# Performance work log

Hardware: AMD Instinct MI355X
Metric: run time of the kernel (lower is better)

The kernel has to match this reference:

```python
import jax, jax.numpy as jnp
import numpy as np

B, S, HID, NH, HD = 2, 2048, 1024, 16, 64  # batch, seq, hidden, heads, head_dim (1024//NH)
ROPE_THETA = 10000.0
EPS = 1e-5


def _ternary_quantize(w):
    # BitNet b1.58 absmean weight quantization: ternary values + scalar scale.
    s = jnp.mean(jnp.abs(w)) + EPS
    q = jnp.clip(jnp.round(w / s), -1.0, 1.0)
    return q, s


def _rotate_half(x):
    x1, x2 = jnp.split(x, 2, axis=-1)
    return jnp.concatenate((-x2, x1), axis=-1)


def _rope_cos_sin(position_ids, head_dim, dtype):
    inv_freq = 1.0 / (ROPE_THETA ** (jnp.arange(0, head_dim, 2, dtype=jnp.float32) / head_dim))
    freqs = position_ids.astype(jnp.float32)[..., None] * inv_freq  # [b, s, hd/2]
    emb = jnp.concatenate((freqs, freqs), axis=-1)  # [b, s, hd]
    # add head axis -> [b, 1, s, hd]
    return jnp.cos(emb)[:, None].astype(dtype), jnp.sin(emb)[:, None].astype(dtype)


def setup_inputs() -> dict:
    key = jax.random.key(0)
    ks = jax.random.split(key, 5)
    hidden_states = jax.random.normal(ks[0], (B, S, HID), jnp.float32)
    hidden_states_scale = jnp.ones((1,), jnp.float32)
    position_ids = jnp.broadcast_to(jnp.arange(S, dtype=jnp.int32), (B, S))
    wq = jax.random.normal(ks[1], (HID, HID), jnp.float32) * 0.02
    wk = jax.random.normal(ks[2], (HID, HID), jnp.float32) * 0.02
    wv = jax.random.normal(ks[3], (HID, HID), jnp.float32) * 0.02
    wo = jax.random.normal(ks[4], (HID, HID), jnp.float32) * 0.02
    return {"hidden_states": hidden_states, "hidden_states_scale": hidden_states_scale,
            "position_ids": position_ids, "wq": wq, "wk": wk, "wv": wv, "wo": wo}


def reference(hidden_states, hidden_states_scale, position_ids, wq, wk, wv, wo):
    b, s, _ = hidden_states.shape
    hs_scale = hidden_states_scale.reshape(())

    # QuantizedLinear: ternary weight values, scale carried separately.
    wq_q, sq = _ternary_quantize(wq)
    wk_q, sk = _ternary_quantize(wk)
    wv_q, sv = _ternary_quantize(wv)
    wo_q, so = _ternary_quantize(wo)

    # Projections in the quantized-value domain: out = x @ Wq^T, out_scale = x_scale * w_scale
    q = jnp.einsum('bsh,oh->bso', hidden_states, wq_q)
    k = jnp.einsum('bsh,oh->bso', hidden_states, wk_q)
    v = jnp.einsum('bsh,oh->bso', hidden_states, wv_q)
    q_scale = hs_scale * sq
    k_scale = hs_scale * sk
    v_scale = hs_scale * sv

    # [b, nh, s, hd]
    q = q.reshape(b, s, NH, HD).transpose(0, 2, 1, 3)
    k = k.reshape(b, s, NH, HD).transpose(0, 2, 1, 3)
    v = v.reshape(b, s, NH, HD).transpose(0, 2, 1, 3)

    cos, sin = _rope_cos_sin(position_ids, HD, q.dtype)
    q = q * cos + _rotate_half(q) * sin
    k = k * cos + _rotate_half(k) * sin

    # quantized_matmul(Q, qs, K, ks): values multiply, scales multiply (scale unused by softmax,
    # matching the original which softmaxes the quantized-domain scores).
    attn = jnp.einsum('bhqd,bhkd->bhqk', q, k).astype(jnp.float32) * (1.0 / np.sqrt(HD))
    attn = jax.nn.softmax(attn, axis=-1)

    # quantized_matmul(attn, 1.0, V, vs)
    out = jnp.einsum('bhqk,bhkd->bhqd', attn, v.astype(jnp.float32))
    out_scale = 1.0 * v_scale

    out = out.transpose(0, 2, 1, 3).reshape(b, s, HID)
    out = jnp.einsum('bsh,oh->bso', out, wo_q)
    out_scale = out_scale * so
    return out, out_scale
```

## Files before the change

kernel.cpp:

```cpp
#include <hip/hip_runtime.h>
#include <hip/hip_bf16.h>

#define NB 2
#define NS 2048
#define NHID 1024
#define NHEAD 16
#define NHD 64
#define NTOK (NB*NS)
#define WELEM (NHID*NHID)

typedef unsigned short u16;
typedef __attribute__((ext_vector_type(4))) float floatx4;
typedef __attribute__((ext_vector_type(16))) float floatx16;
typedef __attribute__((ext_vector_type(8))) __bf16 bf16x8;
typedef __attribute__((ext_vector_type(8))) unsigned short ushort8;
typedef __attribute__((ext_vector_type(4))) unsigned short ushort4v;
typedef __attribute__((ext_vector_type(2))) unsigned uint2v;

__device__ __forceinline__ u16 f2bf(float f) {
  union { float f; unsigned u; } a; a.f = f;
  unsigned u = a.u;
  unsigned r = (u + 0x7fffu + ((u >> 16) & 1u)) >> 16;
  return (u16)r;
}
__device__ __forceinline__ float bf2f(u16 s) {
  union { unsigned u; float f; } a; a.u = ((unsigned)s) << 16;
  return a.f;
}
__device__ __forceinline__ void gload16(const void* g, void* lds) {
  __builtin_amdgcn_global_load_lds(
      (const __attribute__((address_space(1))) unsigned int*)g,
      (__attribute__((address_space(3))) unsigned int*)lds, 16, 0, 0);
}
__device__ __forceinline__ uint2v pl32(unsigned a, unsigned b) {
  return __builtin_amdgcn_permlane32_swap(a, b, false, false);
}
__device__ __forceinline__ float mergemax(float x) {
  uint2v r = pl32(__float_as_uint(x), __float_as_uint(x));
  return fmaxf(__uint_as_float(r[0]), __uint_as_float(r[1]));
}
__device__ __forceinline__ float tmax16(const floatx16& v) {
  float a = fmaxf(fmaxf(v[0], v[1]), v[2]);
  float b = fmaxf(fmaxf(v[3], v[4]), v[5]);
  float c = fmaxf(fmaxf(v[6], v[7]), v[8]);
  float d = fmaxf(fmaxf(v[9], v[10]), v[11]);
  float e = fmaxf(fmaxf(v[12], v[13]), v[14]);
  float r0 = fmaxf(fmaxf(a, b), c);
  float r1 = fmaxf(fmaxf(d, e), v[15]);
  return fmaxf(r0, r1);
}

__global__ void k_abssum(const float* __restrict__ wq, const float* __restrict__ wk,
                         const float* __restrict__ wv, const float* __restrict__ wo,
                         double* __restrict__ sums) {
  const float* srcs[4] = {wq, wk, wv, wo};
  const float* w = srcs[blockIdx.y];
  int idx = (blockIdx.x * 256 + threadIdx.x) * 16;
  float s = 0.f;
#pragma unroll
  for (int j = 0; j < 4; j++) {
    float4 v = *(const float4*)(w + idx + j * 4);
    s += fabsf(v.x) + fabsf(v.y) + fabsf(v.z) + fabsf(v.w);
  }
#pragma unroll
  for (int off = 32; off; off >>= 1) s += __shfl_down(s, off);
  __shared__ float ps[4];
  if ((threadIdx.x & 63) == 0) ps[threadIdx.x >> 6] = s;
  __syncthreads();
  if (threadIdx.x == 0) atomicAdd(&sums[blockIdx.y], (double)(ps[0] + ps[1] + ps[2] + ps[3]));
}

__global__ void k_quantsplit(const float* __restrict__ wq, const float* __restrict__ wk,
                             const float* __restrict__ wv, const float* __restrict__ wo,
                             const double* __restrict__ sums, u16* __restrict__ wt,
                             const float* __restrict__ x,
                             u16* __restrict__ xh, u16* __restrict__ xl,
                             float2* __restrict__ rtab) {
  int bid = blockIdx.x;
  if (bid < 4096) {
    const float* srcs[4] = {wq, wk, wv, wo};
    int y = bid >> 10, xb = bid & 1023;
    const float* w = srcs[y];
    u16* dst = wt + y * WELEM;
    float s = (float)(sums[y] / (double)WELEM) + 1e-5f;
    int idx = (xb * 256 + threadIdx.x) * 4;
    float4 v = *(const float4*)(w + idx);
    float f[4] = {v.x, v.y, v.z, v.w};
    union { u16 ss[4]; uint2 u; } O;
#pragma unroll
    for (int j = 0; j < 4; j++) {
      float q = rintf(f[j] / s);
      q = fminf(1.f, fmaxf(-1.f, q));
      O.ss[j] = f2bf(q);
    }
    *(uint2*)(dst + idx) = O.u;
  } else if (bid < 8192) {
    int idx = ((bid - 4096) * 256 + threadIdx.x) * 4;
    float4 v = *(const float4*)(x + idx);
    float f[4] = {v.x, v.y, v.z, v.w};
    union { u16 s[4]; uint2 u; } H, L;
#pragma unroll
    for (int j = 0; j < 4; j++) {
      u16 hb = f2bf(f[j]);
      H.s[j] = hb;
      L.s[j] = f2bf(f[j] - bf2f(hb));
    }
    *(uint2*)(xh + idx) = H.u;
    *(uint2*)(xl + idx) = L.u;
  } else {
    int idx = (bid - 8192) * 256 + threadIdx.x;
    int d = idx & 31;
    float p = (float)(idx >> 5);
    float inv = exp2f((float)d * -0.4152410118609203f);
    float fr = p * inv;
    rtab[idx] = make_float2(cosf(fr), sinf(fr));
  }
}

template <int MODE>
__global__ __launch_bounds__(256) void k_gemm(
    const u16* __restrict__ Ahi, const u16* __restrict__ Alo,
    const u16* __restrict__ Wt, const int* __restrict__ pos_ids,
    const float2* __restrict__ rtab, float* __restrict__ outf,
    u16* __restrict__ qh, u16* __restrict__ ql,
    u16* __restrict__ kh, u16* __restrict__ kl,
    u16* __restrict__ vt,
    const double* __restrict__ sums, const float* __restrict__ hss) {
  constexpr int BUF = (MODE == 0) ? 24576 : 16384;
  __shared__ __attribute__((aligned(16))) char GSM[2 * BUF];
  const int tid = threadIdx.x;
  const int wave = tid >> 6, lane = tid & 63;
  const int lr = lane & 15, lh = lane >> 4;
  const int bm = blockIdx.x, bn = blockIdx.y, z = blockIdx.z;
  const u16* W = Wt + (MODE == 0 ? z : 3) * WELEM;
  const int wr = wave >> 1, wc = wave & 1;

  floatx4 acc[4][4];
#pragma unroll
  for (int i = 0; i < 4; i++)
#pragma unroll
    for (int j = 0; j < 4; j++) acc[i][j] = (floatx4){0.f, 0.f, 0.f, 0.f};

  const int e0 = tid * 8;
  const int row0 = e0 >> 5, col0 = e0 & 31;

  auto stage = [&](int k0, int nb) {
#pragma unroll
    for (int it = 0; it < 2; ++it) {
      int row = row0 + it * 64;
      gload16(Ahi + (bm * 128 + row) * 1024 + k0 + col0, GSM + nb + it * 4096 + wave * 1024);
      if (MODE == 0 && z != 2)
        gload16(Alo + (bm * 128 + row) * 1024 + k0 + col0, GSM + nb + 8192 + it * 4096 + wave * 1024);
      gload16(W + (bn * 128 + row) * 1024 + k0 + col0,
              GSM + nb + (MODE == 0 ? 16384 : 8192) + it * 4096 + wave * 1024);
    }
  };

  stage(0, 0);

  for (int kt = 0; kt < 32; ++kt) {
    __syncthreads();
    const int cb = (kt & 1) * BUF;
    if (kt < 31) stage((kt + 1) * 32, ((kt + 1) & 1) * BUF);

    const u16* Ahp = (const u16*)(GSM + cb);
    const u16* Bp  = (const u16*)(GSM + cb + (MODE == 0 ? 16384 : 8192));
    bf16x8 ah[4], bfr[4];
#pragma unroll
    for (int mi = 0; mi < 4; mi++)
      ah[mi] = *(const bf16x8*)(Ahp + (wr * 64 + mi * 16 + lr) * 32 + lh * 8);
#pragma unroll
    for (int ni = 0; ni < 4; ni++)
      bfr[ni] = *(const bf16x8*)(Bp + (wc * 64 + ni * 16 + lr) * 32 + lh * 8);
#pragma unroll
    for (int mi = 0; mi < 4; mi++)
#pragma unroll
      for (int ni = 0; ni < 4; ni++)
        acc[mi][ni] = __builtin_amdgcn_mfma_f32_16x16x32_bf16(ah[mi], bfr[ni], acc[mi][ni], 0, 0, 0);
    if (MODE == 0 && z != 2) {
      const u16* Alp = (const u16*)(GSM + cb + 8192);
      bf16x8 al8[4];
#pragma unroll
      for (int mi = 0; mi < 4; mi++)
        al8[mi] = *(const bf16x8*)(Alp + (wr * 64 + mi * 16 + lr) * 32 + lh * 8);
#pragma unroll
      for (int mi = 0; mi < 4; mi++)
#pragma unroll
        for (int ni = 0; ni < 4; ni++)
          acc[mi][ni] = __builtin_amdgcn_mfma_f32_16x16x32_bf16(al8[mi], bfr[ni], acc[mi][ni], 0, 0, 0);
    }
  }

  if (MODE == 1) {
#pragma unroll
    for (int mi = 0; mi < 4; mi++)
#pragma unroll
      for (int ni = 0; ni < 4; ni++)
#pragma unroll
        for (int i = 0; i < 4; i++) {
          int row = bm * 128 + wr * 64 + mi * 16 + lh * 4 + i;
          int col = bn * 128 + wc * 64 + ni * 16 + lr;
          outf[row * 1024 + col] = acc[mi][ni][i];
        }
    if (bm == 0 && bn == 0 && tid == 0) {
      float sv = (float)(sums[2] / (double)WELEM) + 1e-5f;
      float so = (float)(sums[3] / (double)WELEM) + 1e-5f;
      outf[NTOK * NHID] = hss[0] * sv * so;
    }
    return;
  }

  const int hh = bn * 2 + wc;
  if (z == 2) {
#pragma unroll
    for (int mi = 0; mi < 4; mi++) {
      int row0v = bm * 128 + wr * 64 + mi * 16 + lh * 4;
      int bb = row0v >> 11, s_ = row0v & 2047;
      size_t vbase = ((size_t)(bb * NHEAD + hh)) * (NHD * NS) + s_;
#pragma unroll
      for (int ni = 0; ni < 4; ni++) {
        int hd = ni * 16 + lr;
        union { u16 s4[4]; ushort4v v; } V4;
#pragma unroll
        for (int i = 0; i < 4; i++) V4.s4[i] = f2bf(acc[mi][ni][i]);
        *(ushort4v*)(vt + vbase + (size_t)hd * NS) = V4.v;
      }
    }
    return;
  }

  const float qsc = (z == 0) ? 0.125f * 1.4426950408889634f : 1.0f;
  u16* dh = z ? kh : qh;
  u16* dl = z ? kl : ql;
  int posr[4][4];
#pragma unroll
  for (int mi = 0; mi < 4; mi++)
#pragma unroll
    for (int i = 0; i < 4; i++) {
      int row = bm * 128 + wr * 64 + mi * 16 + lh * 4 + i;
      posr[mi][i] = pos_ids[(row >> 11) * NS + (row & 2047)];
    }
#pragma unroll
  for (int ni = 0; ni < 2; ni++) {
    int d = ni * 16 + lr;
#pragma unroll
    for (int mi = 0; mi < 4; mi++)
#pragma unroll
      for (int i = 0; i < 4; i++) {
        int row = bm * 128 + wr * 64 + mi * 16 + lh * 4 + i;
        int bb = row >> 11, s_ = row & 2047;
        float2 cs = rtab[posr[mi][i] * 32 + d];
        float x1 = acc[mi][ni][i], x2 = acc[mi][ni + 2][i];
        float n1 = (x1 * cs.x - x2 * cs.y) * qsc;
        float n2 = (x2 * cs.x + x1 * cs.y) * qsc;
        size_t ob = ((size_t)(bb * NHEAD + hh) * NS + s_) * NHD + d;
        u16 h1 = f2bf(n1);
        dh[ob] = h1;      dl[ob] = f2bf(n1 - bf2f(h1));
        u16 h2 = f2bf(n2);
        dh[ob + 32] = h2; dl[ob + 32] = f2bf(n2 - bf2f(h2));
      }
  }
}

__global__ __launch_bounds__(512) void k_attn(
    const u16* __restrict__ qh, const u16* __restrict__ ql,
    const u16* __restrict__ kh, const u16* __restrict__ kl,
    const u16* __restrict__ vt, u16* __restrict__ aoh) {
  __shared__ __attribute__((aligned(16))) char SM[98304];
  const int tid = threadIdx.x, wave = tid >> 6, lane = tid & 63;
  const int l5 = lane & 31, hi = lane >> 5;
  const int bid = blockIdx.x;
  const int swzb = ((bid & 7) << 5) | (bid >> 3);
  const int qt = swzb & 7, bh = swzb >> 3;
  const int b = bh >> 4, hco = (bh & 15) * NHD;
  const int base = bh * (NS * NHD);
  const int qrow = qt * 256 + wave * 32 + l5;

  bf16x8 qfh[4], qfl[4];
#pragma unroll
  for (int s = 0; s < 4; s++) {
    int off = base + qrow * NHD + s * 16 + hi * 8;
    qfh[s] = *(const bf16x8*)(qh + off);
    qfl[s] = *(const bf16x8*)(ql + off);
  }
  union { ushort8 u; bf16x8 v; } ONES;
#pragma unroll
  for (int j = 0; j < 8; j++) ONES.u[j] = 0x3F80;

  const floatx16 Z16 = {};
  floatx16 acco[2], accl;
  acco[0] = Z16; acco[1] = Z16; accl = Z16;
  float m_r = -1e30f;

  const char* khg0 = (const char*)(kh + base);
  const char* klg0 = (const char*)(kl + base);
  const char* vtg0 = (const char*)(vt + base);

#define STAGE_KV(key0_, nb_)                                                     \
  {                                                                              \
    const char* khg = khg0 + (key0_) * 128;                                      \
    const char* klg = klg0 + (key0_) * 128;                                      \
    const char* vtg = vtg0 + (key0_) * 2;                                        \
    _Pragma("unroll")                                                            \
    for (int it = 0; it < 2; ++it) {                                             \
      int L = it * 8192 + tid * 16;                                              \
      int r7 = (L >> 7) & 7;                                                     \
      int g = L ^ (r7 << 4);                                                     \
      int dst = (nb_) + it * 8192 + wave * 1024;                                 \
      gload16(khg + g, SM + dst);                                                \
      gload16(klg + g, SM + 16384 + dst);                                        \
      int vcol = (L & 255) ^ (((L >> 8) & 15) << 4);                             \
      gload16(vtg + (size_t)(L >> 8) * 4096 + vcol, SM + 32768 + dst);           \
    }                                                                            \
  }

  STAGE_KV(0, 0);

  for (int kt = 0; kt < 16; ++kt) {
    __syncthreads();
    const int cb = (kt & 1) * 49152;
    const int key0 = kt * 128;

    if (kt < 15) STAGE_KV(key0 + 128, ((kt + 1) & 1) * 49152);

    floatx16 sacc[4];
#pragma unroll
    for (int t = 0; t < 4; t++) {
      const int row = 32 * t + l5;
      const int swz = (row & 7) << 4;
      {
        int byt = cb + row * 128 + ((hi * 16) ^ swz);
        bf16x8 ah = *(const bf16x8*)(SM + byt);
        bf16x8 al8 = *(const bf16x8*)(SM + 16384 + byt);
        __builtin_amdgcn_s_setprio(1);
        sacc[t] = __builtin_amdgcn_mfma_f32_32x32x16_bf16(ah, qfh[0], Z16, 0, 0, 0);
        sacc[t] = __builtin_amdgcn_mfma_f32_32x32x16_bf16(ah, qfl[0], sacc[t], 0, 0, 0);
        sacc[t] = __builtin_amdgcn_mfma_f32_32x32x16_bf16(al8, qfh[0], sacc[t], 0, 0, 0);
        __builtin_amdgcn_s_setprio(0);
      }
#pragma unroll
      for (int s = 1; s < 4; s++) {
        int byt = cb + row * 128 + ((s * 32 + hi * 16) ^ swz);
        bf16x8 ah = *(const bf16x8*)(SM + byt);
        bf16x8 al8 = *(const bf16x8*)(SM + 16384 + byt);
        __builtin_amdgcn_s_setprio(1);
        sacc[t] = __builtin_amdgcn_mfma_f32_32x32x16_bf16(ah, qfh[s], sacc[t], 0, 0, 0);
        sacc[t] = __builtin_amdgcn_mfma_f32_32x32x16_bf16(ah, qfl[s], sacc[t], 0, 0, 0);
        sacc[t] = __builtin_amdgcn_mfma_f32_32x32x16_bf16(al8, qfh[s], sacc[t], 0, 0, 0);
        __builtin_amdgcn_s_setprio(0);
      }
    }

    float mt = fmaxf(fmaxf(tmax16(sacc[0]), tmax16(sacc[1])),
                     fmaxf(tmax16(sacc[2]), tmax16(sacc[3])));
    mt = mergemax(mt);
    if (!__all(mt <= m_r + 8.0f)) {
      float mn = fmaxf(m_r, mt);
      float sc2 = exp2f(m_r - mn);
      accl[0] *= sc2;
#pragma unroll
      for (int dt = 0; dt < 2; dt++)
#pragma unroll
        for (int r = 0; r < 16; r++) acco[dt][r] *= sc2;
      m_r = mn;
    }
#pragma unroll
    for (int t = 0; t < 4; t++)
#pragma unroll
      for (int r = 0; r < 16; r++)
        sacc[t][r] = exp2f(sacc[t][r] - m_r);

#pragma unroll
    for (int s = 0; s < 8; s++) {
      int t = s >> 1, rb = (s & 1) * 8;
      union { __bf16 bb[8]; unsigned u[4]; } Wp;
#pragma unroll
      for (int j = 0; j < 8; j++) Wp.bb[j] = (__bf16)sacc[t][rb + j];
      uint2v r02 = pl32(Wp.u[0], Wp.u[2]);
      uint2v r13 = pl32(Wp.u[1], Wp.u[3]);
      union { unsigned u[4]; bf16x8 v; } P;
      P.u[0] = r02[0]; P.u[1] = r13[0]; P.u[2] = r02[1]; P.u[3] = r13[1];
      const int coloff = (s * 32 + hi * 16) ^ ((l5 & 15) << 4);
      bf16x8 v0 = *(const bf16x8*)(SM + cb + 32768 + l5 * 256 + coloff);
      bf16x8 v1 = *(const bf16x8*)(SM + cb + 32768 + (l5 + 32) * 256 + coloff);
      __builtin_amdgcn_s_setprio(1);
      acco[0] = __builtin_amdgcn_mfma_f32_32x32x16_bf16(v0, P.v, acco[0], 0, 0, 0);
      acco[1] = __builtin_amdgcn_mfma_f32_32x32x16_bf16(v1, P.v, acco[1], 0, 0, 0);
      accl    = __builtin_amdgcn_mfma_f32_32x32x16_bf16(ONES.v, P.v, accl, 0, 0, 0);
      __builtin_amdgcn_s_setprio(0);
    }
  }

  float inv = 1.0f / accl[0];
  float* OT = (float*)SM;
#pragma unroll
  for (int rnd = 0; rnd < 2; rnd++) {
    __syncthreads();
    if ((wave >> 2) == rnd) {
      int orow = (wave & 3) * 32 + l5;
#pragma unroll
      for (int dt = 0; dt < 2; dt++)
#pragma unroll
        for (int r = 0; r < 16; r++) {
          int col = (r & 3) + 8 * (r >> 2) + 4 * hi + 32 * dt;
          int cs = (col & 32) | ((col ^ l5) & 31);
          OT[orow * 64 + cs] = acco[dt][r] * inv;
        }
    }
    __syncthreads();
    {
      int row = tid >> 2, q4 = tid & 3;
      union { u16 s8[8]; ushort8 v; } HB[2];
#pragma unroll
      for (int j = 0; j < 16; j++) {
        int c = q4 * 16 + j;
        int cs = (c & 32) | ((c ^ (row & 31)) & 31);
        HB[j >> 3].s8[j & 7] = f2bf(OT[row * 64 + cs]);
      }
      int rowg = qt * 256 + rnd * 128 + row;
      size_t doff = ((size_t)(b * NS + rowg)) * NHID + hco + q4 * 16;
      *(ushort8*)(aoh + doff) = HB[0].v;
      *(ushort8*)(aoh + doff + 8) = HB[1].v;
    }
  }
}

extern "C" void kernel_launch(void* const* d_in, const int* in_sizes, int n_in,
                              void* d_out, int out_size, void* d_ws, size_t ws_size,
                              hipStream_t stream) {
  const float* x   = (const float*)d_in[0];
  const float* hss = (const float*)d_in[1];
  const int*   pos = (const int*)d_in[2];
  const float* wq  = (const float*)d_in[3];
  const float* wk  = (const float*)d_in[4];
  const float* wv  = (const float*)d_in[5];
  const float* wo  = (const float*)d_in[6];
  float* out = (float*)d_out;
  char* ws = (char*)d_ws;
  const size_t MB = 1u << 20;
  u16* wt = (u16*)(ws);
  u16* xh = (u16*)(ws + 8 * MB);
  u16* xl = (u16*)(ws + 16 * MB);
  u16* qh = (u16*)(ws + 24 * MB);
  u16* ql = (u16*)(ws + 32 * MB);
  u16* kh = (u16*)(ws + 40 * MB);
  u16* kl = (u16*)(ws + 48 * MB);
  u16* vt = (u16*)(ws + 56 * MB);
  double* sums = (double*)(ws + 72 * MB);
  float2* rtab = (float2*)(ws + 73 * MB);
  u16* aoh = xh;

  hipMemsetAsync(sums, 0, 4 * sizeof(double), stream);
  k_abssum<<<dim3(256, 4), 256, 0, stream>>>(wq, wk, wv, wo, sums);
  k_quantsplit<<<8448, 256, 0, stream>>>(wq, wk, wv, wo, sums, wt, x, xh, xl, rtab);
  k_gemm<0><<<dim3(32, 8, 3), 256, 0, stream>>>(xh, xl, wt, pos, rtab, nullptr,
                                                qh, ql, kh, kl, vt, nullptr, nullptr);
  k_attn<<<256, 512, 0, stream>>>(qh, ql, kh, kl, vt, aoh);
  k_gemm<1><<<dim3(32, 8, 1), 256, 0, stream>>>(aoh, nullptr, wt, nullptr, nullptr, out,
                                                nullptr, nullptr, nullptr, nullptr, nullptr,
                                                sums, hss);
}
```

Measured before the change: 192.7 us.

## Software-pipeline attention with 64-key tiles and triple-buffered LDS

New measurement: 194.6 us. About the same (+1.0%).

```diff
diff --git a/kernel.cpp b/kernel.cpp
--- a/kernel.cpp
+++ b/kernel.cpp
@@ -266,7 +266,7 @@
     const u16* __restrict__ qh, const u16* __restrict__ ql,
     const u16* __restrict__ kh, const u16* __restrict__ kl,
     const u16* __restrict__ vt, u16* __restrict__ aoh) {
-  __shared__ __attribute__((aligned(16))) char SM[98304];
+  __shared__ __attribute__((aligned(16))) char SM[73728];
   const int tid = threadIdx.x, wave = tid >> 6, lane = tid & 63;
   const int l5 = lane & 31, hi = lane >> 5;
   const int bid = blockIdx.x;
@@ -301,58 +301,46 @@
     const char* khg = khg0 + (key0_) * 128;                                      \
     const char* klg = klg0 + (key0_) * 128;                                      \
     const char* vtg = vtg0 + (key0_) * 2;                                        \
-    _Pragma("unroll")                                                            \
-    for (int it = 0; it < 2; ++it) {                                             \
-      int L = it * 8192 + tid * 16;                                              \
-      int r7 = (L >> 7) & 7;                                                     \
-      int g = L ^ (r7 << 4);                                                     \
-      int dst = (nb_) + it * 8192 + wave * 1024;                                 \
-      gload16(khg + g, SM + dst);                                                \
-      gload16(klg + g, SM + 16384 + dst);                                        \
-      int vcol = (L & 255) ^ (((L >> 8) & 15) << 4);                             \
-      gload16(vtg + (size_t)(L >> 8) * 4096 + vcol, SM + 32768 + dst);           \
-    }                                                                            \
-  }
-
-  STAGE_KV(0, 0);
-
-  for (int kt = 0; kt < 16; ++kt) {
-    __syncthreads();
-    const int cb = (kt & 1) * 49152;
-    const int key0 = kt * 128;
-
-    if (kt < 15) STAGE_KV(key0 + 128, ((kt + 1) & 1) * 49152);
-
-    floatx16 sacc[4];
-#pragma unroll
-    for (int t = 0; t < 4; t++) {
+    int L = tid * 16;                                                            \
+    int r7 = (L >> 7) & 7;                                                       \
+    int g = L ^ (r7 << 4);                                                       \
+    gload16(khg + g, SM + (nb_) + wave * 1024);                                  \
+    gload16(klg + g, SM + (nb_) + 8192 + wave * 1024);                           \
+    int vcol = (L & 127) ^ (r7 << 4);                                            \
+    gload16(vtg + (size_t)(L >> 7) * 4096 + vcol, SM + (nb_) + 16384 + wave * 1024); \
+  }
+
+  auto QK = [&](floatx16 (&sc)[2], int kbuf) {
+#pragma unroll
+    for (int t = 0; t < 2; t++) {
       const int row = 32 * t + l5;
       const int swz = (row & 7) << 4;
       {
-        int byt = cb + row * 128 + ((hi * 16) ^ swz);
+        int byt = kbuf + row * 128 + ((hi * 16) ^ swz);
         bf16x8 ah = *(const bf16x8*)(SM + byt);
-        bf16x8 al8 = *(const bf16x8*)(SM + 16384 + byt);
+        bf16x8 al8 = *(const bf16x8*)(SM + 8192 + byt);
         __builtin_amdgcn_s_setprio(1);
-        sacc[t] = __builtin_amdgcn_mfma_f32_32x32x16_bf16(ah, qfh[0], Z16, 0, 0, 0);
-        sacc[t] = __builtin_amdgcn_mfma_f32_32x32x16_bf16(ah, qfl[0], sacc[t], 0, 0, 0);
-        sacc[t] = __builtin_amdgcn_mfma_f32_32x32x16_bf16(al8, qfh[0], sacc[t], 0, 0, 0);
+        sc[t] = __builtin_amdgcn_mfma_f32_32x32x16_bf16(ah, qfh[0], Z16, 0, 0, 0);
+        sc[t] = __builtin_amdgcn_mfma_f32_32x32x16_bf16(ah, qfl[0], sc[t], 0, 0, 0);
+        sc[t] = __builtin_amdgcn_mfma_f32_32x32x16_bf16(al8, qfh[0], sc[t], 0, 0, 0);
         __builtin_amdgcn_s_setprio(0);
       }
 #pragma unroll
       for (int s = 1; s < 4; s++) {
-        int byt = cb + row * 128 + ((s * 32 + hi * 16) ^ swz);
+        int byt = kbuf + row * 128 + ((s * 32 + hi * 16) ^ swz);
         bf16x8 ah = *(const bf16x8*)(SM + byt);
-        bf16x8 al8 = *(const bf16x8*)(SM + 16384 + byt);
+        bf16x8 al8 = *(const bf16x8*)(SM + 8192 + byt);
         __builtin_amdgcn_s_setprio(1);
-        sacc[t] = __builtin_amdgcn_mfma_f32_32x32x16_bf16(ah, qfh[s], sacc[t], 0, 0, 0);
-        sacc[t] = __builtin_amdgcn_mfma_f32_32x32x16_bf16(ah, qfl[s], sacc[t], 0, 0, 0);
-        sacc[t] = __builtin_amdgcn_mfma_f32_32x32x16_bf16(al8, qfh[s], sacc[t], 0, 0, 0);
+        sc[t] = __builtin_amdgcn_mfma_f32_32x32x16_bf16(ah, qfh[s], sc[t], 0, 0, 0);
+        sc[t] = __builtin_amdgcn_mfma_f32_32x32x16_bf16(ah, qfl[s], sc[t], 0, 0, 0);
+        sc[t] = __builtin_amdgcn_mfma_f32_32x32x16_bf16(al8, qfh[s], sc[t], 0, 0, 0);
         __builtin_amdgcn_s_setprio(0);
       }
     }
-
-    float mt = fmaxf(fmaxf(tmax16(sacc[0]), tmax16(sacc[1])),
-                     fmaxf(tmax16(sacc[2]), tmax16(sacc[3])));
+  };
+
+  auto SMPV = [&](floatx16 (&sc)[2], int vbuf) {
+    float mt = fmaxf(tmax16(sc[0]), tmax16(sc[1]));
     mt = mergemax(mt);
     if (!__all(mt <= m_r + 8.0f)) {
       float mn = fmaxf(m_r, mt);
@@ -365,30 +353,53 @@
       m_r = mn;
     }
 #pragma unroll
-    for (int t = 0; t < 4; t++)
+    for (int t = 0; t < 2; t++)
 #pragma unroll
       for (int r = 0; r < 16; r++)
-        sacc[t][r] = exp2f(sacc[t][r] - m_r);
-
-#pragma unroll
-    for (int s = 0; s < 8; s++) {
+        sc[t][r] = exp2f(sc[t][r] - m_r);
+#pragma unroll
+    for (int s = 0; s < 4; s++) {
       int t = s >> 1, rb = (s & 1) * 8;
       union { __bf16 bb[8]; unsigned u[4]; } Wp;
 #pragma unroll
-      for (int j = 0; j < 8; j++) Wp.bb[j] = (__bf16)sacc[t][rb + j];
+      for (int j = 0; j < 8; j++) Wp.bb[j] = (__bf16)sc[t][rb + j];
       uint2v r02 = pl32(Wp.u[0], Wp.u[2]);
       uint2v r13 = pl32(Wp.u[1], Wp.u[3]);
       union { unsigned u[4]; bf16x8 v; } P;
       P.u[0] = r02[0]; P.u[1] = r13[0]; P.u[2] = r02[1]; P.u[3] = r13[1];
-      const int coloff = (s * 32 + hi * 16) ^ ((l5 & 15) << 4);
-      bf16x8 v0 = *(const bf16x8*)(SM + cb + 32768 + l5 * 256 + coloff);
-      bf16x8 v1 = *(const bf16x8*)(SM + cb + 32768 + (l5 + 32) * 256 + coloff);
+      const int swzv0 = (l5 & 7) << 4;
+      const int coloff = (s * 32 + hi * 16);
+      bf16x8 v0 = *(const bf16x8*)(SM + vbuf + 16384 + l5 * 128 + (coloff ^ swzv0));
+      bf16x8 v1 = *(const bf16x8*)(SM + vbuf + 16384 + (l5 + 32) * 128 + (coloff ^ swzv0));
       __builtin_amdgcn_s_setprio(1);
       acco[0] = __builtin_amdgcn_mfma_f32_32x32x16_bf16(v0, P.v, acco[0], 0, 0, 0);
       acco[1] = __builtin_amdgcn_mfma_f32_32x32x16_bf16(v1, P.v, acco[1], 0, 0, 0);
       accl    = __builtin_amdgcn_mfma_f32_32x32x16_bf16(ONES.v, P.v, accl, 0, 0, 0);
       __builtin_amdgcn_s_setprio(0);
     }
+  };
+
+  floatx16 saccA[2], saccB[2];
+
+  STAGE_KV(0, 0);
+  STAGE_KV(64, 24576);
+  __syncthreads();
+  QK(saccA, 0);
+
+  int b0 = 0, b1 = 24576, b2 = 49152;
+  for (int i = 0; i < 16; ++i) {
+    const int kt = 2 * i;
+    if (i < 15) STAGE_KV((kt + 2) * 64, b2);
+    QK(saccB, b1);
+    SMPV(saccA, b0);
+    __syncthreads();
+    if (i < 15) {
+      STAGE_KV((kt + 3) * 64, b0);
+      QK(saccA, b2);
+    }
+    SMPV(saccB, b1);
+    __syncthreads();
+    int t0 = b0; b0 = b2; b2 = b1; b1 = t0;
   }
 
   float inv = 1.0f / accl[0];
```
